# Performance work log

Measured on AMD Instinct MI355X. Metric: run time of the kernel, lower is better.

## Reference

```python
import jax, jax.numpy as jnp
import numpy as np

FEATURE_SIZES = [300, 1000, 1000, 500, 150, 12, 31, 30, 200, 50000, 50000, 20000, 100000]
# sections per table index i (from feature_sizes_dict -> feature_sections_dict in original)
SECTIONS = [(0, 1), (1, 2), (2, 3), (3, 4), (4, 5), (5, 6), (6, 7), (7, 10),
            (10, 24), (26, 28), (28, 30), (24, 26), (30, 45)]
N, F, E = 8192, 45, 256
_perm, _tbl = [], []
for _i, (_a, _b) in enumerate(SECTIONS):
    for _j in range(_a, _b):
        _perm.append(_j)
        _tbl.append(_i)
PERM = np.array(_perm)              # original Xi column for field position p (concat order)
TBL = np.array(_tbl)                # table index for field position p
OFFSETS = np.concatenate([[0], np.cumsum(FEATURE_SIZES)[:-1]]).astype(np.int32)
FIELD_OFF = OFFSETS[TBL]            # row offset into concatenated table per field position
TOTAL_V = int(np.sum(FEATURE_SIZES))  # 223273
VOCAB_COL = np.zeros(F, np.int32)
VOCAB_COL[PERM] = np.array(FEATURE_SIZES, np.int32)[TBL]  # per-column valid vocab for Xi


def setup_inputs() -> dict:
    key = jax.random.key(0)
    ks = jax.random.split(key, 10)
    Xi = jax.random.randint(ks[0], (N, F), 0, jnp.asarray(VOCAB_COL), dtype=jnp.int32)
    Xv = jax.random.uniform(ks[1], (N, F), dtype=jnp.float32)
    W1 = jax.random.normal(ks[2], (TOTAL_V, 1), dtype=jnp.float32) * 0.01
    W2 = jax.random.normal(ks[3], (TOTAL_V, E), dtype=jnp.float32) * 0.01
    bias = jax.random.normal(ks[4], (1,), dtype=jnp.float32)
    l1_w = jax.random.normal(ks[5], (32, F * E), dtype=jnp.float32) * 0.02
    l1_b = jnp.zeros((32,), jnp.float32)
    l2_w = jax.random.normal(ks[6], (32, 32), dtype=jnp.float32) * 0.02
    l2_b = jnp.zeros((32,), jnp.float32)
    return {"Xi": Xi, "Xv": Xv, "W1": W1, "W2": W2, "bias": bias,
            "l1_w": l1_w, "l1_b": l1_b, "bn1_g": jnp.ones((32,), jnp.float32),
            "bn1_b": jnp.zeros((32,), jnp.float32), "l2_w": l2_w, "l2_b": l2_b,
            "bn2_g": jnp.ones((32,), jnp.float32), "bn2_b": jnp.zeros((32,), jnp.float32)}


def _batchnorm(x, g, b, eps=1e-5):
    # training-mode BN: biased batch statistics (PyTorch normalization convention)
    m = x.mean(0)
    v = x.var(0)
    return (x - m) * jax.lax.rsqrt(v + eps) * g + b


def reference(Xi, Xv, W1, W2, bias, l1_w, l1_b, bn1_g, bn1_b, l2_w, l2_b, bn2_g, bn2_b):
    perm = jnp.asarray(PERM)
    foff = jnp.asarray(FIELD_OFF)
    idx = Xi[:, perm] + foff[None, :]          # (N, 45) rows into concatenated tables
    xv = Xv[:, perm]                            # (N, 45) values in concat order
    # first-order: scalar embedding * value per field
    fm_first = W1[idx, 0] * xv                  # (N, 45)
    # second-order: E-dim embedding * value per field
    e = W2[idx] * xv[:, :, None]                # (N, 45, E)
    s = e.sum(axis=1)                           # (N, E)
    fm_second = 0.5 * (s * s - (e * e).sum(axis=1))  # (N, E)
    # deep part (concat of per-field 2nd-order embs, in original loop order)
    deep = e.reshape(e.shape[0], -1)            # (N, 45*E)
    h = _batchnorm(deep @ l1_w.T + l1_b, bn1_g, bn1_b)
    h = _batchnorm(h @ l2_w.T + l2_b, bn2_g, bn2_b)  # (N, 32); no final num_classes linear in original
    return fm_first.sum(axis=1) + fm_second.sum(axis=1) + h.sum(axis=1) + bias  # (N,)
```

## Files before the change

### kernel.cpp

```cpp
#include <hip/hip_runtime.h>
#include <hip/hip_bf16.h>

#define NS 8192
#define NF 45
#define ED 256
#define L1K 11520
#define NH 32

typedef __attribute__((ext_vector_type(8))) short bf16x8;
typedef __attribute__((ext_vector_type(4))) float f32x4;
typedef __attribute__((ext_vector_type(4))) unsigned uint32x4;

__constant__ int c_perm[NF] = {
    0,1,2,3,4,5,6,7,8,9,
    10,11,12,13,14,15,16,17,18,19,20,21,22,23,
    26,27, 28,29, 24,25,
    30,31,32,33,34,35,36,37,38,39,40,41,42,43,44};
__constant__ int c_foff[NF] = {
    0,300,1300,2300,2800,2950,2962,2993,2993,2993,
    3023,3023,3023,3023,3023,3023,3023,3023,3023,3023,3023,3023,3023,3023,
    3223,3223, 53223,53223, 103223,103223,
    123223,123223,123223,123223,123223,123223,123223,123223,
    123223,123223,123223,123223,123223,123223,123223};

__device__ __forceinline__ short f2bf(float x) {
    unsigned u = __builtin_bit_cast(unsigned, x);
    u += 0x7fffu + ((u >> 16) & 1u);
    return (short)(u >> 16);
}

__device__ __forceinline__ unsigned pk_bf16(float a, float b) {
    unsigned r;
    asm("v_cvt_pk_bf16_f32 %0, %1, %2" : "=v"(r) : "v"(a), "v"(b));
    return r;
}

__global__ __launch_bounds__(256) void k_pack(const float* __restrict__ l1w,
                                              short* __restrict__ bfrag) {
    int t = blockIdx.x * 256 + threadIdx.x;
    if (t >= NF * 8192) return;
    int i  = t & 7;
    int l  = (t >> 3) & 63;
    int nt = (t >> 9) & 1;
    int ks = (t >> 10) & 7;
    int f  = t >> 13;
    int kout = nt * 16 + (l & 15);
    int col  = f * 256 + ks * 32 + (l >> 4) * 8 + i;
    bfrag[t] = f2bf(l1w[kout * L1K + col]);
}

__global__ __launch_bounds__(256) void k_main(const float* __restrict__ W2,
                                              const float* __restrict__ W1,
                                              const int* __restrict__ Xi,
                                              const float* __restrict__ Xv,
                                              const short* __restrict__ bfrag,
                                              float* __restrict__ h1h,
                                              float* __restrict__ parth) {
    __shared__ int   s_idx[16 * NF];
    __shared__ float s_xv [16 * NF];
    __shared__ float s_red[4 * 16 * NH];
    __shared__ float s_q[4][16];
    __shared__ float s_fm1[16];

    const int tid  = threadIdx.x;
    const int w    = tid >> 6;
    const int l    = tid & 63;
    const int m    = l & 15;
    const int g4   = l >> 4;
    const int half = blockIdx.x & 1;
    const int n0   = (blockIdx.x >> 1) * 16;
    const int ks   = half * 4 + w;

    for (int t = tid; t < 16 * NF; t += 256) {
        int f = t % NF;
        int n = n0 + t / NF;
        int col = c_perm[f];
        s_idx[t] = Xi[n * NF + col] + c_foff[f];
        s_xv[t]  = Xv[n * NF + col];
    }
    __syncthreads();

    f32x4 acc0 = {0.f, 0.f, 0.f, 0.f};
    f32x4 acc1 = {0.f, 0.f, 0.f, 0.f};
    float sA[8];
    #pragma unroll
    for (int i = 0; i < 8; ++i) sA[i] = 0.f;
    float esq = 0.f, fm1 = 0.f;

    const short* bbase = bfrag + (size_t)ks * 1024 + l * 8;
    const float* wbase = W2 + ks * 32 + g4 * 8;
    const bool  isw0   = (half == 0 && w == 0);

    int   idx_c = s_idx[m * NF + 0];
    float xv_c  = s_xv [m * NF + 0];
    const float* wr0 = wbase + (size_t)idx_c * ED;
    f32x4  a0_c = *(const f32x4*)(wr0);
    f32x4  a1_c = *(const f32x4*)(wr0 + 4);
    bf16x8 b0_c = *(const bf16x8*)(bbase);
    bf16x8 b1_c = *(const bf16x8*)(bbase + 512);
    float  w1_c = isw0 ? W1[idx_c] : 0.f;

    for (int f = 0; f < NF; ++f) {
        f32x4  a0_n, a1_n;
        bf16x8 b0_n, b1_n;
        float  xv_n, w1_n;
        const bool more = (f + 1 < NF);
        if (more) {
            int idx_n = s_idx[m * NF + f + 1];
            xv_n = s_xv[m * NF + f + 1];
            const float* wr = wbase + (size_t)idx_n * ED;
            a0_n = *(const f32x4*)(wr);
            a1_n = *(const f32x4*)(wr + 4);
            const short* bp = bbase + (size_t)(f + 1) * 8192;
            b0_n = *(const bf16x8*)(bp);
            b1_n = *(const bf16x8*)(bp + 512);
            w1_n = isw0 ? W1[idx_n] : 0.f;
        }

        float e[8];
        e[0] = a0_c.x * xv_c; e[1] = a0_c.y * xv_c;
        e[2] = a0_c.z * xv_c; e[3] = a0_c.w * xv_c;
        e[4] = a1_c.x * xv_c; e[5] = a1_c.y * xv_c;
        e[6] = a1_c.z * xv_c; e[7] = a1_c.w * xv_c;

        #pragma unroll
        for (int i = 0; i < 8; ++i) { sA[i] += e[i]; esq += e[i] * e[i]; }

        uint32x4 au;
        au.x = pk_bf16(e[0], e[1]);
        au.y = pk_bf16(e[2], e[3]);
        au.z = pk_bf16(e[4], e[5]);
        au.w = pk_bf16(e[6], e[7]);
        bf16x8 Af = __builtin_bit_cast(bf16x8, au);

        acc0 = __builtin_amdgcn_mfma_f32_16x16x32_bf16(Af, b0_c, acc0, 0, 0, 0);
        acc1 = __builtin_amdgcn_mfma_f32_16x16x32_bf16(Af, b1_c, acc1, 0, 0, 0);

        fm1 += w1_c * xv_c;

        if (more) {
            a0_c = a0_n; a1_c = a1_n;
            b0_c = b0_n; b1_c = b1_n;
            xv_c = xv_n; w1_c = w1_n;
        }
    }

    float q = -esq;
    #pragma unroll
    for (int i = 0; i < 8; ++i) q += sA[i] * sA[i];
    q += __shfl_xor(q, 16);
    q += __shfl_xor(q, 32);
    if (l < 16) s_q[w][l] = q;
    if (w == 0 && l < 16) s_fm1[l] = fm1;

    #pragma unroll
    for (int r = 0; r < 4; ++r) {
        s_red[w * 512 + (g4 * 4 + r) * 32 +      m] = acc0[r];
        s_red[w * 512 + (g4 * 4 + r) * 32 + 16 + m] = acc1[r];
    }
    __syncthreads();

    float* h1out = h1h + (size_t)half * NS * NH;
    for (int t = tid; t < 512; t += 256) {
        float v = s_red[t] + s_red[512 + t] + s_red[1024 + t] + s_red[1536 + t];
        h1out[(size_t)n0 * NH + t] = v;
    }
    if (tid < 16) {
        float fm2 = 0.5f * (s_q[0][tid] + s_q[1][tid] + s_q[2][tid] + s_q[3][tid]);
        parth[half * NS + n0 + tid] = s_fm1[tid] + fm2;
    }
}

__global__ __launch_bounds__(256) void k_stats(const float* __restrict__ h1h,
                                               float* __restrict__ S1,
                                               float* __restrict__ S2) {
    __shared__ float hc[128 * NH];
    const int tid = threadIdx.x;
    const int base = blockIdx.x * 128;
    for (int t = tid; t < 128 * NH; t += 256)
        hc[t] = h1h[(size_t)base * NH + t] + h1h[(size_t)NS * NH + base * NH + t];
    __syncthreads();

    const int j = tid >> 3;
    const int ks = (tid & 7) * 4;
    float a0 = 0.f, a1 = 0.f, a2 = 0.f, a3 = 0.f;
    for (int n = 0; n < 128; ++n) {
        float hj = hc[n * NH + j];
        f32x4 h = *(const f32x4*)&hc[n * NH + ks];
        a0 += hj * h.x; a1 += hj * h.y; a2 += hj * h.z; a3 += hj * h.w;
    }
    atomicAdd(&S2[j * NH + ks + 0], a0);
    atomicAdd(&S2[j * NH + ks + 1], a1);
    atomicAdd(&S2[j * NH + ks + 2], a2);
    atomicAdd(&S2[j * NH + ks + 3], a3);
    if (tid < NH) {
        float s = 0.f;
        for (int n = 0; n < 128; ++n) s += hc[n * NH + tid];
        atomicAdd(&S1[tid], s);
    }
}

__global__ __launch_bounds__(256) void k_coef(const float* __restrict__ S1,
                                              const float* __restrict__ S2,
                                              const float* __restrict__ g1,
                                              const float* __restrict__ l2w,
                                              const float* __restrict__ g2,
                                              const float* __restrict__ b2,
                                              const float* __restrict__ bias,
                                              float* __restrict__ cvec,
                                              float* __restrict__ k0out) {
    __shared__ float m1[NH], d1[NH], g2r2[NH], csh[NH];
    const int t = threadIdx.x;
    const float invN = 1.f / (float)NS;
    if (t < NH) {
        float mm = S1[t] * invN;
        float v1 = S2[t * NH + t] * invN - mm * mm;
        m1[t] = mm;
        d1[t] = g1[t] * rsqrtf(v1 + 1e-5f);
    }
    __syncthreads();
    if (t < NH) {
        float aw[NH];
        float p = 0.f;
        for (int j = 0; j < NH; ++j) { aw[j] = l2w[t * NH + j] * d1[j]; p += aw[j] * m1[j]; }
        float v2 = 0.f;
        for (int j = 0; j < NH; ++j) {
            float acc = 0.f;
            for (int j2 = 0; j2 < NH; ++j2) acc += aw[j2] * S2[j * NH + j2];
            v2 += aw[j] * acc;
        }
        v2 = v2 * invN - p * p;
        g2r2[t] = g2[t] * rsqrtf(v2 + 1e-5f);
    }
    __syncthreads();
    if (t < NH) {
        float s = 0.f;
        for (int k = 0; k < NH; ++k) s += g2r2[k] * l2w[k * NH + t];
        float c = d1[t] * s;
        csh[t] = c;
        cvec[t] = c;
    }
    __syncthreads();
    if (t == 0) {
        float k0 = bias[0];
        for (int k = 0; k < NH; ++k) k0 += b2[k];
        for (int j = 0; j < NH; ++j) k0 -= csh[j] * m1[j];
        k0out[0] = k0;
    }
}

__global__ __launch_bounds__(256) void k_final(const float* __restrict__ h1h,
                                               const float* __restrict__ parth,
                                               const float* __restrict__ cvec,
                                               const float* __restrict__ k0p,
                                               float* __restrict__ out) {
    __shared__ float c[NH];
    __shared__ float k0s;
    const int t = threadIdx.x;
    if (t < NH) c[t] = cvec[t];
    if (t == 0) k0s = k0p[0];
    __syncthreads();
    const int n = blockIdx.x * 256 + t;
    const f32x4* hp0 = (const f32x4*)(h1h + (size_t)n * NH);
    const f32x4* hp1 = (const f32x4*)(h1h + (size_t)NS * NH + (size_t)n * NH);
    float dot = 0.f;
    #pragma unroll
    for (int q = 0; q < 8; ++q) {
        f32x4 h0 = hp0[q];
        f32x4 h1 = hp1[q];
        dot += (h0.x + h1.x) * c[q * 4]     + (h0.y + h1.y) * c[q * 4 + 1]
             + (h0.z + h1.z) * c[q * 4 + 2] + (h0.w + h1.w) * c[q * 4 + 3];
    }
    out[n] = parth[n] + parth[NS + n] + dot + k0s;
}

extern "C" void kernel_launch(void* const* d_in, const int* in_sizes, int n_in,
                              void* d_out, int out_size, void* d_ws, size_t ws_size,
                              hipStream_t stream) {
    const int*   Xi   = (const int*)  d_in[0];
    const float* Xv   = (const float*)d_in[1];
    const float* W1   = (const float*)d_in[2];
    const float* W2   = (const float*)d_in[3];
    const float* bias = (const float*)d_in[4];
    const float* l1w  = (const float*)d_in[5];
    const float* g1   = (const float*)d_in[7];
    const float* l2w  = (const float*)d_in[9];
    const float* g2   = (const float*)d_in[11];
    const float* b2   = (const float*)d_in[12];
    float* out = (float*)d_out;

    char* ws = (char*)d_ws;
    short* bfrag = (short*)ws;
    float* h1h   = (float*)(ws + (size_t)368640 * 2);
    float* parth = h1h + (size_t)2 * NS * NH;
    float* S1    = parth + 2 * NS;
    float* S2    = S1 + NH;
    float* cvec  = S2 + NH * NH;
    float* k0p   = cvec + NH;

    hipMemsetAsync(S1, 0, (NH + NH * NH) * sizeof(float), stream);
    k_pack <<<(NF * 8192 + 255) / 256, 256, 0, stream>>>(l1w, bfrag);
    k_main <<<NS / 16 * 2, 256, 0, stream>>>(W2, W1, Xi, Xv, bfrag, h1h, parth);
    k_stats<<<64, 256, 0, stream>>>(h1h, S1, S2);
    k_coef <<<1, 256, 0, stream>>>(S1, S2, g1, l2w, g2, b2, bias, cvec, k0p);
    k_final<<<NS / 256, 256, 0, stream>>>(h1h, parth, cvec, k0p, out);
}
```

Before: 380.4 us.

## Deepen gather prefetch to three fields, add occupancy hint, split stats, cache S2

The main kernel's field loop now keeps three fields of W2 rows and bfrag fragments in flight instead of one, to hide gather latency, and gains a launch bound minimum of 4 blocks per CU. The stats kernel uses 128 blocks of 64 rows instead of 64 blocks of 128 rows for more parallelism, at the cost of more atomics. The coefficient kernel stages S2 in shared memory before its nested loops. The deeper prefetch raises register pressure, which the occupancy hint may turn into spills.

```diff
diff --git a/kernel.cpp b/kernel.cpp
--- a/kernel.cpp
+++ b/kernel.cpp
@@ -49,13 +49,13 @@
     bfrag[t] = f2bf(l1w[kout * L1K + col]);
 }
 
-__global__ __launch_bounds__(256) void k_main(const float* __restrict__ W2,
-                                              const float* __restrict__ W1,
-                                              const int* __restrict__ Xi,
-                                              const float* __restrict__ Xv,
-                                              const short* __restrict__ bfrag,
-                                              float* __restrict__ h1h,
-                                              float* __restrict__ parth) {
+__global__ __launch_bounds__(256, 4) void k_main(const float* __restrict__ W2,
+                                                 const float* __restrict__ W1,
+                                                 const int* __restrict__ Xi,
+                                                 const float* __restrict__ Xv,
+                                                 const short* __restrict__ bfrag,
+                                                 float* __restrict__ h1h,
+                                                 float* __restrict__ parth) {
     __shared__ int   s_idx[16 * NF];
     __shared__ float s_xv [16 * NF];
     __shared__ float s_red[4 * 16 * NH];
@@ -90,60 +90,62 @@
     const short* bbase = bfrag + (size_t)ks * 1024 + l * 8;
     const float* wbase = W2 + ks * 32 + g4 * 8;
     const bool  isw0   = (half == 0 && w == 0);
-
-    int   idx_c = s_idx[m * NF + 0];
-    float xv_c  = s_xv [m * NF + 0];
-    const float* wr0 = wbase + (size_t)idx_c * ED;
-    f32x4  a0_c = *(const f32x4*)(wr0);
-    f32x4  a1_c = *(const f32x4*)(wr0 + 4);
-    bf16x8 b0_c = *(const bf16x8*)(bbase);
-    bf16x8 b1_c = *(const bf16x8*)(bbase + 512);
-    float  w1_c = isw0 ? W1[idx_c] : 0.f;
-
-    for (int f = 0; f < NF; ++f) {
-        f32x4  a0_n, a1_n;
-        bf16x8 b0_n, b1_n;
-        float  xv_n, w1_n;
-        const bool more = (f + 1 < NF);
-        if (more) {
-            int idx_n = s_idx[m * NF + f + 1];
-            xv_n = s_xv[m * NF + f + 1];
-            const float* wr = wbase + (size_t)idx_n * ED;
-            a0_n = *(const f32x4*)(wr);
-            a1_n = *(const f32x4*)(wr + 4);
-            const short* bp = bbase + (size_t)(f + 1) * 8192;
-            b0_n = *(const bf16x8*)(bp);
-            b1_n = *(const bf16x8*)(bp + 512);
-            w1_n = isw0 ? W1[idx_n] : 0.f;
-        }
-
-        float e[8];
-        e[0] = a0_c.x * xv_c; e[1] = a0_c.y * xv_c;
-        e[2] = a0_c.z * xv_c; e[3] = a0_c.w * xv_c;
-        e[4] = a1_c.x * xv_c; e[5] = a1_c.y * xv_c;
-        e[6] = a1_c.z * xv_c; e[7] = a1_c.w * xv_c;
-
-        #pragma unroll
-        for (int i = 0; i < 8; ++i) { sA[i] += e[i]; esq += e[i] * e[i]; }
-
-        uint32x4 au;
-        au.x = pk_bf16(e[0], e[1]);
-        au.y = pk_bf16(e[2], e[3]);
-        au.z = pk_bf16(e[4], e[5]);
-        au.w = pk_bf16(e[6], e[7]);
-        bf16x8 Af = __builtin_bit_cast(bf16x8, au);
-
-        acc0 = __builtin_amdgcn_mfma_f32_16x16x32_bf16(Af, b0_c, acc0, 0, 0, 0);
-        acc1 = __builtin_amdgcn_mfma_f32_16x16x32_bf16(Af, b1_c, acc1, 0, 0, 0);
-
-        fm1 += w1_c * xv_c;
-
-        if (more) {
-            a0_c = a0_n; a1_c = a1_n;
-            b0_c = b0_n; b1_c = b1_n;
-            xv_c = xv_n; w1_c = w1_n;
-        }
-    }
+    const int   mNF    = m * NF;
+
+#define LOADF(ff, A0, A1, B0, B1, XV, W1R)                          \
+    do {                                                            \
+        int idx_ = s_idx[mNF + (ff)];                               \
+        XV = s_xv[mNF + (ff)];                                      \
+        const float* wr_ = wbase + (size_t)idx_ * ED;               \
+        A0 = *(const f32x4*)(wr_);                                  \
+        A1 = *(const f32x4*)(wr_ + 4);                              \
+        const short* bp_ = bbase + (size_t)(ff) * 8192;             \
+        B0 = *(const bf16x8*)(bp_);                                 \
+        B1 = *(const bf16x8*)(bp_ + 512);                           \
+        W1R = isw0 ? W1[idx_] : 0.f;                                \
+    } while (0)
+
+#define COMPF(A0, A1, B0, B1, XV, W1R)                              \
+    do {                                                            \
+        float e0 = A0.x * XV, e1 = A0.y * XV, e2 = A0.z * XV, e3 = A0.w * XV; \
+        float e4 = A1.x * XV, e5 = A1.y * XV, e6 = A1.z * XV, e7 = A1.w * XV; \
+        sA[0] += e0; sA[1] += e1; sA[2] += e2; sA[3] += e3;         \
+        sA[4] += e4; sA[5] += e5; sA[6] += e6; sA[7] += e7;         \
+        esq += e0 * e0; esq += e1 * e1; esq += e2 * e2; esq += e3 * e3; \
+        esq += e4 * e4; esq += e5 * e5; esq += e6 * e6; esq += e7 * e7; \
+        uint32x4 au_;                                               \
+        au_.x = pk_bf16(e0, e1);                                    \
+        au_.y = pk_bf16(e2, e3);                                    \
+        au_.z = pk_bf16(e4, e5);                                    \
+        au_.w = pk_bf16(e6, e7);                                    \
+        bf16x8 Af_ = __builtin_bit_cast(bf16x8, au_);               \
+        acc0 = __builtin_amdgcn_mfma_f32_16x16x32_bf16(Af_, B0, acc0, 0, 0, 0); \
+        acc1 = __builtin_amdgcn_mfma_f32_16x16x32_bf16(Af_, B1, acc1, 0, 0, 0); \
+        fm1 += W1R * XV;                                            \
+    } while (0)
+
+    f32x4  A0a, A1a, A0b, A1b, A0c, A1c;
+    bf16x8 B0a, B1a, B0b, B1b, B0c, B1c;
+    float  XVa, XVb, XVc, W1a, W1b, W1c;
+
+    LOADF(0, A0a, A1a, B0a, B1a, XVa, W1a);
+    LOADF(1, A0b, A1b, B0b, B1b, XVb, W1b);
+    LOADF(2, A0c, A1c, B0c, B1c, XVc, W1c);
+
+    for (int f = 0; f < NF - 3; f += 3) {
+        COMPF(A0a, A1a, B0a, B1a, XVa, W1a);
+        LOADF(f + 3, A0a, A1a, B0a, B1a, XVa, W1a);
+        COMPF(A0b, A1b, B0b, B1b, XVb, W1b);
+        LOADF(f + 4, A0b, A1b, B0b, B1b, XVb, W1b);
+        COMPF(A0c, A1c, B0c, B1c, XVc, W1c);
+        LOADF(f + 5, A0c, A1c, B0c, B1c, XVc, W1c);
+    }
+    COMPF(A0a, A1a, B0a, B1a, XVa, W1a);
+    COMPF(A0b, A1b, B0b, B1b, XVb, W1b);
+    COMPF(A0c, A1c, B0c, B1c, XVc, W1c);
+
+#undef LOADF
+#undef COMPF
 
     float q = -esq;
     #pragma unroll
@@ -174,17 +176,17 @@
 __global__ __launch_bounds__(256) void k_stats(const float* __restrict__ h1h,
                                                float* __restrict__ S1,
                                                float* __restrict__ S2) {
-    __shared__ float hc[128 * NH];
+    __shared__ float hc[64 * NH];
     const int tid = threadIdx.x;
-    const int base = blockIdx.x * 128;
-    for (int t = tid; t < 128 * NH; t += 256)
+    const int base = blockIdx.x * 64;
+    for (int t = tid; t < 64 * NH; t += 256)
         hc[t] = h1h[(size_t)base * NH + t] + h1h[(size_t)NS * NH + base * NH + t];
     __syncthreads();
 
     const int j = tid >> 3;
     const int ks = (tid & 7) * 4;
     float a0 = 0.f, a1 = 0.f, a2 = 0.f, a3 = 0.f;
-    for (int n = 0; n < 128; ++n) {
+    for (int n = 0; n < 64; ++n) {
         float hj = hc[n * NH + j];
         f32x4 h = *(const f32x4*)&hc[n * NH + ks];
         a0 += hj * h.x; a1 += hj * h.y; a2 += hj * h.z; a3 += hj * h.w;
@@ -195,7 +197,7 @@
     atomicAdd(&S2[j * NH + ks + 3], a3);
     if (tid < NH) {
         float s = 0.f;
-        for (int n = 0; n < 128; ++n) s += hc[n * NH + tid];
+        for (int n = 0; n < 64; ++n) s += hc[n * NH + tid];
         atomicAdd(&S1[tid], s);
     }
 }
@@ -210,11 +212,14 @@
                                               float* __restrict__ cvec,
                                               float* __restrict__ k0out) {
     __shared__ float m1[NH], d1[NH], g2r2[NH], csh[NH];
+    __shared__ float s2s[NH * NH];
     const int t = threadIdx.x;
     const float invN = 1.f / (float)NS;
+    for (int i = t; i < NH * NH; i += 256) s2s[i] = S2[i];
+    __syncthreads();
     if (t < NH) {
         float mm = S1[t] * invN;
-        float v1 = S2[t * NH + t] * invN - mm * mm;
+        float v1 = s2s[t * NH + t] * invN - mm * mm;
         m1[t] = mm;
         d1[t] = g1[t] * rsqrtf(v1 + 1e-5f);
     }
@@ -226,7 +231,7 @@
         float v2 = 0.f;
         for (int j = 0; j < NH; ++j) {
             float acc = 0.f;
-            for (int j2 = 0; j2 < NH; ++j2) acc += aw[j2] * S2[j * NH + j2];
+            for (int j2 = 0; j2 < NH; ++j2) acc += aw[j2] * s2s[j * NH + j2];
             v2 += aw[j] * acc;
         }
         v2 = v2 * invN - p * p;
@@ -301,7 +306,7 @@
     hipMemsetAsync(S1, 0, (NH + NH * NH) * sizeof(float), stream);
     k_pack <<<(NF * 8192 + 255) / 256, 256, 0, stream>>>(l1w, bfrag);
     k_main <<<NS / 16 * 2, 256, 0, stream>>>(W2, W1, Xi, Xv, bfrag, h1h, parth);
-    k_stats<<<64, 256, 0, stream>>>(h1h, S1, S2);
+    k_stats<<<128, 256, 0, stream>>>(h1h, S1, S2);
     k_coef <<<1, 256, 0, stream>>>(S1, S2, g1, l2w, g2, b2, bias, cvec, k0p);
     k_final<<<NS / 256, 256, 0, stream>>>(h1h, parth, cvec, k0p, out);
 }
```

Measured after the change: 380.7 us. No clear change (+0.1%).
